# Kernel tuning notes

Hardware: AMD Instinct MI355X
Metric: run time of the kernel (lower is better)

## Reference

```python
import jax, jax.numpy as jnp
import numpy as np

IN, H, T = 16, 64, 25

def _lstm_layer(x, w_ih, w_hh, b_ih, b_hh):
    # x: [B,T,I]; w_ih: [4H,I]; w_hh: [4H,H]; biases: [4H]
    B = x.shape[0]
    x_proj = jnp.einsum('bti,gi->btg', x, w_ih) + b_ih + b_hh  # [B,T,4H]
    h0 = jnp.zeros((B, H), x.dtype)
    c0 = jnp.zeros((B, H), x.dtype)
    def step(carry, xt):
        h, c = carry
        gates = xt + h @ w_hh.T  # [B,4H]
        i, f, g, o = jnp.split(gates, 4, axis=-1)  # torch gate order i,f,g,o
        i = jax.nn.sigmoid(i); f = jax.nn.sigmoid(f)
        g = jnp.tanh(g);       o = jax.nn.sigmoid(o)
        c = f * c + i * g
        h = o * jnp.tanh(c)
        return (h, c), h
    _, hs = jax.lax.scan(step, (h0, c0), jnp.swapaxes(x_proj, 0, 1))  # [T,B,H]
    return jnp.swapaxes(hs, 0, 1)  # [B,T,H]


def setup_inputs() -> dict:
    key = jax.random.key(0)
    ks = jax.random.split(key, 20)
    s = 1.0 / np.sqrt(H)
    u = lambda k, shp: jax.random.uniform(k, shp, jnp.float32, -s, s)
    inp = {
        'x': jax.random.normal(ks[0], (32768, T, IN), jnp.float32),
        'w_ih0': u(ks[1], (4 * H, IN)), 'w_hh0': u(ks[2], (4 * H, H)),
        'b_ih0': u(ks[3], (4 * H,)),    'b_hh0': u(ks[4], (4 * H,)),
        'w_ih1': u(ks[5], (4 * H, H)),  'w_hh1': u(ks[6], (4 * H, H)),
        'b_ih1': u(ks[7], (4 * H,)),    'b_hh1': u(ks[8], (4 * H,)),
        'fc1_w': u(ks[9],  (128, H * T)), 'fc1_b': u(ks[10], (128,)),
        'fc2_w': u(ks[11], (128, H * T)), 'fc2_b': u(ks[12], (128,)),
        'fc3_w': u(ks[13], (128, H * T)), 'fc3_b': u(ks[14], (128,)),
        'l1_w': u(ks[15], (5, 128)),  'l1_b': u(ks[16], (5,)),
        'l2_w': u(ks[17], (4, 128)),  'l2_b': u(ks[18], (4,)),
        'l3_w': u(ks[19], (8, 128)),  'l3_b': jnp.zeros((8,), jnp.float32),
    }
    return inp


def reference(x, w_ih0, w_hh0, b_ih0, b_hh0, w_ih1, w_hh1, b_ih1, b_hh1,
              fc1_w, fc1_b, fc2_w, fc2_b, fc3_w, fc3_b,
              l1_w, l1_b, l2_w, l2_b, l3_w, l3_b):
    out = _lstm_layer(x, w_ih0, w_hh0, b_ih0, b_hh0)
    out = _lstm_layer(out, w_ih1, w_hh1, b_ih1, b_hh1)  # [B,T,H]
    flat = out.reshape(out.shape[0], -1)  # [B, T*H]
    x1 = jax.nn.relu(flat @ fc1_w.T + fc1_b)
    x2 = jax.nn.relu(flat @ fc2_w.T + fc2_b)
    x3 = jax.nn.relu(flat @ fc3_w.T + fc3_b)
    o1 = x1 @ l1_w.T + l1_b
    o2 = x2 @ l2_w.T + l2_b
    o3 = x3 @ l3_w.T + l3_b
    return (o1, o2, o3)
```

## Files before the change

### kernel.cpp

```cpp
#include <hip/hip_runtime.h>
#include <stdint.h>

#define BATCH 32768
#define TT    25

typedef float f32x4 __attribute__((ext_vector_type(4)));
typedef short s16x8 __attribute__((ext_vector_type(8)));

__device__ __align__(16) short g_Wc[384 * 1600];

#define LOG2E 1.442695040888963f

__device__ __forceinline__ uint32_t f2bf(float v){
  uint32_t u = __float_as_uint(v);
  return (u + 0x7fffu + ((u >> 16) & 1u)) >> 16;
}
__device__ __forceinline__ short f2bfs(float v){ return (short)f2bf(v); }

__device__ __forceinline__ uint32_t cvt_pk_bf16(float lo, float hi){
  uint32_t d;
  asm("v_cvt_pk_bf16_f32 %0, %1, %2" : "=v"(d) : "v"(lo), "v"(hi));
  return d;
}

__device__ __forceinline__ float sigm(float x){
  float e = __builtin_amdgcn_exp2f(-LOG2E * x);
  return __builtin_amdgcn_rcpf(1.0f + e);
}
__device__ __forceinline__ float tanh_(float x){
  float e = __builtin_amdgcn_exp2f(-2.0f*LOG2E * x);
  return 2.0f*__builtin_amdgcn_rcpf(1.0f + e) - 1.0f;
}
__device__ __forceinline__ s16x8 pack8(float4 a, float4 b){
  s16x8 v;
  v[0]=f2bfs(a.x); v[1]=f2bfs(a.y); v[2]=f2bfs(a.z); v[3]=f2bfs(a.w);
  v[4]=f2bfs(b.x); v[5]=f2bfs(b.y); v[6]=f2bfs(b.z); v[7]=f2bfs(b.w);
  return v;
}

__global__ void conv_wc_kernel(const float* __restrict__ fc1w,
                               const float* __restrict__ fc2w,
                               const float* __restrict__ fc3w){
  const int j = blockIdx.x;
  const float* src = (j < 128) ? fc1w + j*1600
                   : (j < 256) ? fc2w + (j-128)*1600
                               : fc3w + (j-256)*1600;
  for (int k = threadIdx.x; k < 1600; k += 256)
    g_Wc[j*1600 + k] = f2bfs(src[k]);
}

__global__ __launch_bounds__(512, 1) void lstm2_mfma_kernel(
    const float* __restrict__ x,
    const float* __restrict__ wih0, const float* __restrict__ whh0,
    const float* __restrict__ bih0, const float* __restrict__ bhh0,
    const float* __restrict__ wih1, const float* __restrict__ whh1,
    const float* __restrict__ bih1, const float* __restrict__ bhh1,
    short* __restrict__ flat)
{
  __shared__ short Abuf[4*64*64];
  char* const Ab = (char*)Abuf;

  const int tid  = threadIdx.x;
  const int lane = tid & 63;
  const int wv   = tid >> 6;
  const int w4   = wv & 3;
  const int wg   = wv >> 2;
  const int lrow = lane & 15;
  const int lk   = lane >> 4;
  const int sw   = (lrow & 7) << 4;
  const int sb   = blockIdx.x * 64;
  const int u    = w4*16 + lrow;

  {
    s16x8 z = {0,0,0,0,0,0,0,0};
    int idx = tid * 32;
    char* pz = Ab + ((idx < 8192) ? 8192 + idx : 16384 + idx);
    *(s16x8*)pz = z; *(s16x8*)(pz + 16) = z;
  }

  s16x8 W1f[4][4], B0x[4], B0h[4][2];
  #pragma unroll
  for (int n = 0; n < 4; n++){
    const int g = n*64 + u;
    #pragma unroll
    for (int kt = 0; kt < 4; kt++){
      const float* src = (kt < 2 ? wih1 + g*64 + kt*32 : whh1 + g*64 + (kt-2)*32) + lk*8;
      W1f[n][kt] = pack8(*(const float4*)src, *(const float4*)(src+4));
    }
    if (lk < 2){
      const float* src = wih0 + g*16 + lk*8;
      B0x[n] = pack8(*(const float4*)src, *(const float4*)(src+4));
    } else {
      s16x8 z = {0,0,0,0,0,0,0,0}; B0x[n] = z;
    }
    #pragma unroll
    for (int kt = 0; kt < 2; kt++){
      const float* src = whh0 + g*64 + kt*32 + lk*8;
      B0h[n][kt] = pack8(*(const float4*)src, *(const float4*)(src+4));
    }
  }

  float b0v[4], b1v[4];
  #pragma unroll
  for (int n = 0; n < 4; n++){
    b0v[n] = bih0[n*64+u] + bhh0[n*64+u];
    b1v[n] = bih1[n*64+u] + bhh1[n*64+u];
  }

  const float* xbase[2];
  #pragma unroll
  for (int m = 0; m < 2; m++)
    xbase[m] = x + (size_t)(sb + wg*32 + m*16 + lrow)*(TT*16) + (lk&1)*8;
  s16x8 xf[2];
  #pragma unroll
  for (int m = 0; m < 2; m++)
    xf[m] = pack8(*(const float4*)(xbase[m]), *(const float4*)(xbase[m] + 4));

  float c0[2][4], c1[2][4];
  #pragma unroll
  for (int m = 0; m < 2; m++)
    #pragma unroll
    for (int r = 0; r < 4; r++){ c0[m][r] = 0.f; c1[m][r] = 0.f; }

  __syncthreads();

  #pragma unroll 1
  for (int t = 0; t < TT; t++){
    const int p  = t & 1;
    const int pn = p ^ 1;
    f32x4 acc[2][4];
    #pragma unroll
    for (int m = 0; m < 2; m++)
      #pragma unroll
      for (int n = 0; n < 4; n++){ f32x4 iv = {b0v[n],b0v[n],b0v[n],b0v[n]}; acc[m][n] = iv; }
    #pragma unroll
    for (int m = 0; m < 2; m++)
      #pragma unroll
      for (int n = 0; n < 4; n++)
        acc[m][n] = __builtin_amdgcn_mfma_f32_16x16x32_bf16(xf[m], B0x[n], acc[m][n], 0, 0, 0);
    #pragma unroll
    for (int kt = 0; kt < 2; kt++){
      s16x8 a[2];
      #pragma unroll
      for (int m = 0; m < 2; m++){
        int row = wg*32 + m*16 + lrow;
        a[m] = *(const s16x8*)(Ab + pn*8192 + row*128 + ((kt*64 + lk*16) ^ sw));
      }
      #pragma unroll
      for (int m = 0; m < 2; m++)
        #pragma unroll
        for (int n = 0; n < 4; n++)
          acc[m][n] = __builtin_amdgcn_mfma_f32_16x16x32_bf16(a[m], B0h[n][kt], acc[m][n], 0, 0, 0);
    }
    short hb[2][4];
    #pragma unroll
    for (int m = 0; m < 2; m++)
      #pragma unroll
      for (int r = 0; r < 4; r++){
        float iv = sigm(acc[m][0][r]);
        float fv = sigm(acc[m][1][r]);
        float gv = tanh_(acc[m][2][r]);
        float ov = sigm(acc[m][3][r]);
        float c  = fmaf(fv, c0[m][r], iv*gv); c0[m][r] = c;
        hb[m][r] = f2bfs(ov * tanh_(c));
      }
    #pragma unroll
    for (int m = 0; m < 2; m++)
      #pragma unroll
      for (int r = 0; r < 4; r++){
        int mine = (int)(uint16_t)hb[m][r];
        int part = __shfl_xor(mine, 1);
        if ((lane & 1) == 0){
          int s_ = wg*32 + m*16 + lk*4 + r;
          uint32_t pk = (uint32_t)mine | ((uint32_t)part << 16);
          *(uint32_t*)(Ab + p*8192 + s_*128 + ((u*2) ^ ((s_&7)<<4))) = pk;
        }
      }
    __syncthreads();

    s16x8 xfn[2];
    if (t + 1 < TT){
      #pragma unroll
      for (int m = 0; m < 2; m++)
        xfn[m] = pack8(*(const float4*)(xbase[m] + (t+1)*16),
                       *(const float4*)(xbase[m] + (t+1)*16 + 4));
    }
    #pragma unroll
    for (int m = 0; m < 2; m++)
      #pragma unroll
      for (int n = 0; n < 4; n++){ f32x4 iv = {b1v[n],b1v[n],b1v[n],b1v[n]}; acc[m][n] = iv; }
    #pragma unroll
    for (int kt = 0; kt < 4; kt++){
      const int reg = (kt < 2) ? p*8192 : 16384 + pn*8192;
      const int ko  = (kt & 1) * 64;
      s16x8 a[2];
      #pragma unroll
      for (int m = 0; m < 2; m++){
        int row = wg*32 + m*16 + lrow;
        a[m] = *(const s16x8*)(Ab + reg + row*128 + ((ko + lk*16) ^ sw));
      }
      #pragma unroll
      for (int m = 0; m < 2; m++)
        #pragma unroll
        for (int n = 0; n < 4; n++)
          acc[m][n] = __builtin_amdgcn_mfma_f32_16x16x32_bf16(a[m], W1f[n][kt], acc[m][n], 0, 0, 0);
    }
    #pragma unroll
    for (int m = 0; m < 2; m++)
      #pragma unroll
      for (int r = 0; r < 4; r++){
        float iv = sigm(acc[m][0][r]);
        float fv = sigm(acc[m][1][r]);
        float gv = tanh_(acc[m][2][r]);
        float ov = sigm(acc[m][3][r]);
        float c  = fmaf(fv, c1[m][r], iv*gv); c1[m][r] = c;
        hb[m][r] = f2bfs(ov * tanh_(c));
      }
    #pragma unroll
    for (int m = 0; m < 2; m++)
      #pragma unroll
      for (int r = 0; r < 4; r++){
        int mine = (int)(uint16_t)hb[m][r];
        int part = __shfl_xor(mine, 1);
        if ((lane & 1) == 0){
          int s_ = wg*32 + m*16 + lk*4 + r;
          uint32_t pk = (uint32_t)mine | ((uint32_t)part << 16);
          *(uint32_t*)(Ab + 16384 + p*8192 + s_*128 + ((u*2) ^ ((s_&7)<<4))) = pk;
          *(uint32_t*)(flat + (size_t)(sb+s_)*1600 + t*64 + u) = pk;
        }
      }
    __syncthreads();
    #pragma unroll
    for (int m = 0; m < 2; m++) xf[m] = xfn[m];
  }
}

__global__ __launch_bounds__(256,1) void fc_mfma_kernel(
    const short* __restrict__ flat,
    const float* __restrict__ fc1b, const float* __restrict__ fc2b, const float* __restrict__ fc3b,
    const float* __restrict__ l1w,  const float* __restrict__ l1b,
    const float* __restrict__ l2w,  const float* __restrict__ l2b,
    const float* __restrict__ l3w,  const float* __restrict__ l3b,
    float* __restrict__ out)
{
  __shared__ short Rs[64*384];
  char* const Rb = (char*)Rs;
  const int tid  = threadIdx.x;
  const int lane = tid & 63;
  const int wv   = tid >> 6;
  const int lrow = lane & 15;
  const int lk   = lane >> 4;
  const int sb   = blockIdx.x * 64;

  f32x4 acc[4][6];
  #pragma unroll
  for (int n = 0; n < 6; n++){
    int j = wv*96 + n*16 + lrow;
    float bv = (j < 128) ? fc1b[j] : (j < 256) ? fc2b[j-128] : fc3b[j-256];
    #pragma unroll
    for (int m = 0; m < 4; m++){ f32x4 iv = {bv,bv,bv,bv}; acc[m][n] = iv; }
  }

  const char* Abase = (const char*)(flat + (size_t)sb*1600);
  const char* Bbase = (const char*)g_Wc;
  #pragma unroll 1
  for (int kc = 0; kc < 50; kc++){
    s16x8 a[4], b[6];
    #pragma unroll
    for (int m = 0; m < 4; m++)
      a[m] = *(const s16x8*)(Abase + (size_t)(m*16+lrow)*3200 + kc*64 + lk*16);
    #pragma unroll
    for (int n = 0; n < 6; n++)
      b[n] = *(const s16x8*)(Bbase + (size_t)(wv*96+n*16+lrow)*3200 + kc*64 + lk*16);
    #pragma unroll
    for (int m = 0; m < 4; m++)
      #pragma unroll
      for (int n = 0; n < 6; n++)
        acc[m][n] = __builtin_amdgcn_mfma_f32_16x16x32_bf16(a[m], b[n], acc[m][n], 0, 0, 0);
  }

  #pragma unroll
  for (int m = 0; m < 4; m++)
    #pragma unroll
    for (int n = 0; n < 6; n++)
      #pragma unroll
      for (int r = 0; r < 4; r++){
        float v  = fmaxf(acc[m][n][r], 0.f);
        float vp = __shfl_xor(v, 1);
        uint32_t pk = cvt_pk_bf16(v, vp);
        if ((lane & 1) == 0){
          int s_ = m*16 + lk*4 + r;
          int fc = wv*96 + n*16 + lrow;
          *(uint32_t*)(Rb + s_*768 + ((fc*2) ^ ((s_&7)<<4))) = pk;
        }
      }
  __syncthreads();

  const float* Lw[3] = {l1w, l2w, l3w};
  const int   odim[3] = {5, 4, 8};
  s16x8 Bh[3][4];
  #pragma unroll
  for (int q = 0; q < 3; q++){
    #pragma unroll
    for (int kt = 0; kt < 4; kt++){
      if (lrow < odim[q]){
        const float* src = Lw[q] + lrow*128 + kt*32 + lk*8;
        Bh[q][kt] = pack8(*(const float4*)src, *(const float4*)(src+4));
      } else {
        s16x8 z = {0,0,0,0,0,0,0,0}; Bh[q][kt] = z;
      }
    }
  }
  f32x4 acc2[4][3];
  {
    float bv0 = (lrow < 5) ? l1b[lrow] : 0.f;
    float bv1 = (lrow < 4) ? l2b[lrow] : 0.f;
    float bv2 = (lrow < 8) ? l3b[lrow] : 0.f;
    #pragma unroll
    for (int m = 0; m < 4; m++){
      f32x4 i0 = {bv0,bv0,bv0,bv0}; acc2[m][0] = i0;
      f32x4 i1 = {bv1,bv1,bv1,bv1}; acc2[m][1] = i1;
      f32x4 i2 = {bv2,bv2,bv2,bv2}; acc2[m][2] = i2;
    }
  }
  #pragma unroll
  for (int q = 0; q < 3; q++){
    #pragma unroll
    for (int kt = 0; kt < 4; kt++){
      s16x8 a[4];
      #pragma unroll
      for (int m = 0; m < 4; m++){
        int row = m*16 + lrow;
        a[m] = *(const s16x8*)(Rb + row*768 + ((q*256 + kt*64 + lk*16) ^ ((row&7)<<4)));
      }
      #pragma unroll
      for (int m = 0; m < 4; m++)
        acc2[m][q] = __builtin_amdgcn_mfma_f32_16x16x32_bf16(a[m], Bh[q][kt], acc2[m][q], 0, 0, 0);
    }
  }
  #pragma unroll
  for (int m = 0; m < 4; m++)
    #pragma unroll
    for (int r = 0; r < 4; r++){
      int smp = sb + m*16 + lk*4 + r;
      if (lrow < 5) out[(size_t)smp*5 + lrow] = acc2[m][0][r];
      if (lrow < 4) out[(size_t)BATCH*5 + (size_t)smp*4 + lrow] = acc2[m][1][r];
      if (lrow < 8) out[(size_t)BATCH*9 + (size_t)smp*8 + lrow] = acc2[m][2][r];
    }
}

extern "C" void kernel_launch(void* const* d_in, const int* in_sizes, int n_in,
                              void* d_out, int out_size, void* d_ws, size_t ws_size,
                              hipStream_t stream)
{
  const float* x    = (const float*)d_in[0];
  const float* wih0 = (const float*)d_in[1];
  const float* whh0 = (const float*)d_in[2];
  const float* bih0 = (const float*)d_in[3];
  const float* bhh0 = (const float*)d_in[4];
  const float* wih1 = (const float*)d_in[5];
  const float* whh1 = (const float*)d_in[6];
  const float* bih1 = (const float*)d_in[7];
  const float* bhh1 = (const float*)d_in[8];
  const float* fc1w = (const float*)d_in[9];
  const float* fc1b = (const float*)d_in[10];
  const float* fc2w = (const float*)d_in[11];
  const float* fc2b = (const float*)d_in[12];
  const float* fc3w = (const float*)d_in[13];
  const float* fc3b = (const float*)d_in[14];
  const float* l1w  = (const float*)d_in[15];
  const float* l1b  = (const float*)d_in[16];
  const float* l2w  = (const float*)d_in[17];
  const float* l2b  = (const float*)d_in[18];
  const float* l3w  = (const float*)d_in[19];
  const float* l3b  = (const float*)d_in[20];

  float* out  = (float*)d_out;
  short* flat = (short*)d_ws;
  if (ws_size < (size_t)BATCH*1600*2) return;

  conv_wc_kernel<<<dim3(384), dim3(256), 0, stream>>>(fc1w, fc2w, fc3w);

  lstm2_mfma_kernel<<<dim3(BATCH/64), dim3(512), 0, stream>>>(
      x, wih0, whh0, bih0, bhh0, wih1, whh1, bih1, bhh1, flat);

  fc_mfma_kernel<<<dim3(BATCH/64), dim3(256), 0, stream>>>(
      flat, fc1b, fc2b, fc3b, l1w, l1b, l2w, l2b, l3w, l3b, out);
}
```

Baseline: 381.6 us.

## Wavefront-pipeline LSTM layers so layer0 step t+1 overlaps layer1 step t

Restructures the recurrent loop into a skewed pipeline. Layer 0's first step is peeled, and each iteration then computes layer 1 at step k alongside layer 0 at step k+1. Both sets of MFMAs are independent and are interleaved, with one barrier per iteration instead of two. This is meant to halve synchronisation and give more MFMA-level parallelism to hide latency. In exchange it uses more registers for two accumulator sets, and the zero-init of the LDS region now assumes at least 256 threads.

```diff
diff --git a/kernel.cpp b/kernel.cpp
--- a/kernel.cpp
+++ b/kernel.cpp
@@ -73,9 +73,10 @@
 
   {
     s16x8 z = {0,0,0,0,0,0,0,0};
-    int idx = tid * 32;
-    char* pz = Ab + ((idx < 8192) ? 8192 + idx : 16384 + idx);
-    *(s16x8*)pz = z; *(s16x8*)(pz + 16) = z;
+    if (tid < 256){
+      char* pz = Ab + 24576 + tid*32;
+      *(s16x8*)pz = z; *(s16x8*)(pz + 16) = z;
+    }
   }
 
   s16x8 W1f[4][4], B0x[4], B0h[4][2];
@@ -111,127 +112,156 @@
   #pragma unroll
   for (int m = 0; m < 2; m++)
     xbase[m] = x + (size_t)(sb + wg*32 + m*16 + lrow)*(TT*16) + (lk&1)*8;
-  s16x8 xf[2];
+
+  float c0[2][4], c1[2][4];
   #pragma unroll
   for (int m = 0; m < 2; m++)
-    xf[m] = pack8(*(const float4*)(xbase[m]), *(const float4*)(xbase[m] + 4));
-
-  float c0[2][4], c1[2][4];
-  #pragma unroll
-  for (int m = 0; m < 2; m++)
     #pragma unroll
     for (int r = 0; r < 4; r++){ c0[m][r] = 0.f; c1[m][r] = 0.f; }
 
-  __syncthreads();
-
-  #pragma unroll 1
-  for (int t = 0; t < TT; t++){
-    const int p  = t & 1;
-    const int pn = p ^ 1;
-    f32x4 acc[2][4];
-    #pragma unroll
-    for (int m = 0; m < 2; m++)
-      #pragma unroll
-      for (int n = 0; n < 4; n++){ f32x4 iv = {b0v[n],b0v[n],b0v[n],b0v[n]}; acc[m][n] = iv; }
+  {
+    s16x8 x0[2];
+    #pragma unroll
+    for (int m = 0; m < 2; m++)
+      x0[m] = pack8(*(const float4*)(xbase[m]), *(const float4*)(xbase[m] + 4));
+    f32x4 a0[2][4];
+    #pragma unroll
+    for (int m = 0; m < 2; m++)
+      #pragma unroll
+      for (int n = 0; n < 4; n++){ f32x4 iv = {b0v[n],b0v[n],b0v[n],b0v[n]}; a0[m][n] = iv; }
     #pragma unroll
     for (int m = 0; m < 2; m++)
       #pragma unroll
       for (int n = 0; n < 4; n++)
-        acc[m][n] = __builtin_amdgcn_mfma_f32_16x16x32_bf16(xf[m], B0x[n], acc[m][n], 0, 0, 0);
-    #pragma unroll
-    for (int kt = 0; kt < 2; kt++){
-      s16x8 a[2];
-      #pragma unroll
-      for (int m = 0; m < 2; m++){
-        int row = wg*32 + m*16 + lrow;
-        a[m] = *(const s16x8*)(Ab + pn*8192 + row*128 + ((kt*64 + lk*16) ^ sw));
-      }
-      #pragma unroll
-      for (int m = 0; m < 2; m++)
-        #pragma unroll
-        for (int n = 0; n < 4; n++)
-          acc[m][n] = __builtin_amdgcn_mfma_f32_16x16x32_bf16(a[m], B0h[n][kt], acc[m][n], 0, 0, 0);
-    }
-    short hb[2][4];
+        a0[m][n] = __builtin_amdgcn_mfma_f32_16x16x32_bf16(x0[m], B0x[n], a0[m][n], 0, 0, 0);
     #pragma unroll
     for (int m = 0; m < 2; m++)
       #pragma unroll
       for (int r = 0; r < 4; r++){
-        float iv = sigm(acc[m][0][r]);
-        float fv = sigm(acc[m][1][r]);
-        float gv = tanh_(acc[m][2][r]);
-        float ov = sigm(acc[m][3][r]);
-        float c  = fmaf(fv, c0[m][r], iv*gv); c0[m][r] = c;
-        hb[m][r] = f2bfs(ov * tanh_(c));
-      }
-    #pragma unroll
-    for (int m = 0; m < 2; m++)
-      #pragma unroll
-      for (int r = 0; r < 4; r++){
-        int mine = (int)(uint16_t)hb[m][r];
+        float iv = sigm(a0[m][0][r]);
+        float fv = sigm(a0[m][1][r]);
+        float gv = tanh_(a0[m][2][r]);
+        float ov = sigm(a0[m][3][r]);
+        float c  = iv*gv; c0[m][r] = c;
+        int mine = (int)(uint16_t)f2bfs(ov * tanh_(c));
         int part = __shfl_xor(mine, 1);
         if ((lane & 1) == 0){
           int s_ = wg*32 + m*16 + lk*4 + r;
           uint32_t pk = (uint32_t)mine | ((uint32_t)part << 16);
-          *(uint32_t*)(Ab + p*8192 + s_*128 + ((u*2) ^ ((s_&7)<<4))) = pk;
+          *(uint32_t*)(Ab + 0*8192 + s_*128 + ((u*2) ^ ((s_&7)<<4))) = pk;
         }
       }
-    __syncthreads();
-
-    s16x8 xfn[2];
-    if (t + 1 < TT){
-      #pragma unroll
-      for (int m = 0; m < 2; m++)
-        xfn[m] = pack8(*(const float4*)(xbase[m] + (t+1)*16),
-                       *(const float4*)(xbase[m] + (t+1)*16 + 4));
-    }
-    #pragma unroll
-    for (int m = 0; m < 2; m++)
-      #pragma unroll
-      for (int n = 0; n < 4; n++){ f32x4 iv = {b1v[n],b1v[n],b1v[n],b1v[n]}; acc[m][n] = iv; }
-    #pragma unroll
-    for (int kt = 0; kt < 4; kt++){
-      const int reg = (kt < 2) ? p*8192 : 16384 + pn*8192;
-      const int ko  = (kt & 1) * 64;
-      s16x8 a[2];
+  }
+  s16x8 xf[2];
+  #pragma unroll
+  for (int m = 0; m < 2; m++)
+    xf[m] = pack8(*(const float4*)(xbase[m] + 16), *(const float4*)(xbase[m] + 16 + 4));
+
+  __syncthreads();
+
+  #pragma unroll 1
+  for (int k = 0; k < TT; k++){
+    const int p  = k & 1;
+    const int pn = p ^ 1;
+    const bool doL0 = (k + 1 < TT);
+
+    s16x8 a0f[2][2], a1f[2][2];
+    #pragma unroll
+    for (int kt = 0; kt < 2; kt++)
       #pragma unroll
       for (int m = 0; m < 2; m++){
         int row = wg*32 + m*16 + lrow;
-        a[m] = *(const s16x8*)(Ab + reg + row*128 + ((ko + lk*16) ^ sw));
-      }
+        a0f[m][kt] = *(const s16x8*)(Ab + p*8192 + row*128 + ((kt*64 + lk*16) ^ sw));
+        a1f[m][kt] = *(const s16x8*)(Ab + 16384 + pn*8192 + row*128 + ((kt*64 + lk*16) ^ sw));
+      }
+
+    s16x8 xfn[2];
+    if (k + 2 < TT){
+      #pragma unroll
+      for (int m = 0; m < 2; m++)
+        xfn[m] = pack8(*(const float4*)(xbase[m] + (k+2)*16),
+                       *(const float4*)(xbase[m] + (k+2)*16 + 4));
+    }
+
+    f32x4 acc1[2][4], acc0[2][4];
+    #pragma unroll
+    for (int m = 0; m < 2; m++)
+      #pragma unroll
+      for (int n = 0; n < 4; n++){
+        f32x4 i1 = {b1v[n],b1v[n],b1v[n],b1v[n]}; acc1[m][n] = i1;
+        f32x4 i0 = {b0v[n],b0v[n],b0v[n],b0v[n]}; acc0[m][n] = i0;
+      }
+    #pragma unroll
+    for (int kt = 0; kt < 2; kt++)
       #pragma unroll
       for (int m = 0; m < 2; m++)
         #pragma unroll
         for (int n = 0; n < 4; n++)
-          acc[m][n] = __builtin_amdgcn_mfma_f32_16x16x32_bf16(a[m], W1f[n][kt], acc[m][n], 0, 0, 0);
-    }
+          acc1[m][n] = __builtin_amdgcn_mfma_f32_16x16x32_bf16(a0f[m][kt], W1f[n][kt], acc1[m][n], 0, 0, 0);
+    if (doL0){
+      #pragma unroll
+      for (int m = 0; m < 2; m++)
+        #pragma unroll
+        for (int n = 0; n < 4; n++)
+          acc0[m][n] = __builtin_amdgcn_mfma_f32_16x16x32_bf16(xf[m], B0x[n], acc0[m][n], 0, 0, 0);
+    }
+    #pragma unroll
+    for (int kt = 0; kt < 2; kt++)
+      #pragma unroll
+      for (int m = 0; m < 2; m++)
+        #pragma unroll
+        for (int n = 0; n < 4; n++)
+          acc1[m][n] = __builtin_amdgcn_mfma_f32_16x16x32_bf16(a1f[m][kt], W1f[n][kt+2], acc1[m][n], 0, 0, 0);
+    if (doL0){
+      #pragma unroll
+      for (int kt = 0; kt < 2; kt++)
+        #pragma unroll
+        for (int m = 0; m < 2; m++)
+          #pragma unroll
+          for (int n = 0; n < 4; n++)
+            acc0[m][n] = __builtin_amdgcn_mfma_f32_16x16x32_bf16(a0f[m][kt], B0h[n][kt], acc0[m][n], 0, 0, 0);
+    }
+
     #pragma unroll
     for (int m = 0; m < 2; m++)
       #pragma unroll
       for (int r = 0; r < 4; r++){
-        float iv = sigm(acc[m][0][r]);
-        float fv = sigm(acc[m][1][r]);
-        float gv = tanh_(acc[m][2][r]);
-        float ov = sigm(acc[m][3][r]);
+        float iv = sigm(acc1[m][0][r]);
+        float fv = sigm(acc1[m][1][r]);
+        float gv = tanh_(acc1[m][2][r]);
+        float ov = sigm(acc1[m][3][r]);
         float c  = fmaf(fv, c1[m][r], iv*gv); c1[m][r] = c;
-        hb[m][r] = f2bfs(ov * tanh_(c));
-      }
-    #pragma unroll
-    for (int m = 0; m < 2; m++)
-      #pragma unroll
-      for (int r = 0; r < 4; r++){
-        int mine = (int)(uint16_t)hb[m][r];
+        int mine = (int)(uint16_t)f2bfs(ov * tanh_(c));
         int part = __shfl_xor(mine, 1);
         if ((lane & 1) == 0){
           int s_ = wg*32 + m*16 + lk*4 + r;
           uint32_t pk = (uint32_t)mine | ((uint32_t)part << 16);
           *(uint32_t*)(Ab + 16384 + p*8192 + s_*128 + ((u*2) ^ ((s_&7)<<4))) = pk;
-          *(uint32_t*)(flat + (size_t)(sb+s_)*1600 + t*64 + u) = pk;
+          *(uint32_t*)(flat + (size_t)(sb+s_)*1600 + k*64 + u) = pk;
         }
       }
+    if (doL0){
+      #pragma unroll
+      for (int m = 0; m < 2; m++)
+        #pragma unroll
+        for (int r = 0; r < 4; r++){
+          float iv = sigm(acc0[m][0][r]);
+          float fv = sigm(acc0[m][1][r]);
+          float gv = tanh_(acc0[m][2][r]);
+          float ov = sigm(acc0[m][3][r]);
+          float c  = fmaf(fv, c0[m][r], iv*gv); c0[m][r] = c;
+          int mine = (int)(uint16_t)f2bfs(ov * tanh_(c));
+          int part = __shfl_xor(mine, 1);
+          if ((lane & 1) == 0){
+            int s_ = wg*32 + m*16 + lk*4 + r;
+            uint32_t pk = (uint32_t)mine | ((uint32_t)part << 16);
+            *(uint32_t*)(Ab + pn*8192 + s_*128 + ((u*2) ^ ((s_&7)<<4))) = pk;
+          }
+        }
+      #pragma unroll
+      for (int m = 0; m < 2; m++) xf[m] = xfn[m];
+    }
     __syncthreads();
-    #pragma unroll
-    for (int m = 0; m < 2; m++) xf[m] = xfn[m];
   }
 }
 
```

Measured after the change: 581.7 us. 1.52x slower.
